# Kernel optimization log

Measured on AMD Instinct MI355X. Metric: run time of the kernel, lower is better.

The kernel has to match this reference:

```python
import jax, jax.numpy as jnp
import numpy as np

EMBED = 512
HEADS = 1
HEAD_DIM = EMBED // HEADS  # 512 (heads must be 1 for the original torch code to run)
N, S = 4, 4096


def setup_inputs() -> dict:
    key = jax.random.key(0)
    ks = jax.random.split(key, 9)
    scale = 1.0 / np.sqrt(EMBED)
    return {
        "values": jax.random.normal(ks[0], (N, 1, S, EMBED), dtype=jnp.float32),
        "keys": jax.random.normal(ks[1], (N, 1, S, EMBED), dtype=jnp.float32),
        "query": jax.random.normal(ks[2], (N, 1, S, EMBED), dtype=jnp.float32),
        "mask": jax.random.randint(ks[3], (N, 1, S, S), 0, 2, dtype=jnp.int32),
        "Wv": jax.random.normal(ks[4], (EMBED, EMBED), dtype=jnp.float32) * scale,
        "Wk": jax.random.normal(ks[5], (EMBED, EMBED), dtype=jnp.float32) * scale,
        "Wq": jax.random.normal(ks[6], (EMBED, EMBED), dtype=jnp.float32) * scale,
        "Wo": jax.random.normal(ks[7], (EMBED, EMBED), dtype=jnp.float32) * scale,
        "bo": jnp.zeros((EMBED,), dtype=jnp.float32),
    }


def reference(values, keys, query, mask, Wv, Wk, Wq, Wo, bo):
    n = query.shape[0]
    q_len = query.shape[2]
    # reshape(N, -1, heads, head_dim); inputs are [N, 1, S, E] -> [N, S, H, Dh]
    v = values.reshape(n, -1, HEADS, HEAD_DIM)
    k = keys.reshape(n, -1, HEADS, HEAD_DIM)
    q = query.reshape(n, -1, HEADS, HEAD_DIM)
    # per-module linear projections (nn.Linear: y = x @ W.T)
    v = jnp.einsum('nlhd,ed->nlhe', v, Wv)
    k = jnp.einsum('nlhd,ed->nlhe', k, Wk)
    q = jnp.einsum('nqhd,ed->nqhe', q, Wq)
    # full [N, H, Q, K] score matrix, as in the original
    energy = jnp.einsum('nqhd,nkhd->nhqk', q, k)
    energy = jnp.where(mask == 0, jnp.float32(-1e20), energy)
    attn = jax.nn.softmax(energy / np.sqrt(HEAD_DIM), axis=3)
    out = jnp.einsum('nhql,nlhd->nqhd', attn, v).reshape(n, q_len, HEADS * HEAD_DIM)
    return out @ Wo.T + bo
```

## Files before the change

kernel.cpp:

```cpp
#include <hip/hip_runtime.h>

typedef __bf16 bf16x8 __attribute__((ext_vector_type(8)));
typedef __bf16 bf16x4 __attribute__((ext_vector_type(4)));
typedef float f32x4 __attribute__((ext_vector_type(4)));
typedef float f32x16 __attribute__((ext_vector_type(16)));

#define MFMA16(a, b, c) __builtin_amdgcn_mfma_f32_16x16x32_bf16((a), (b), (c), 0, 0, 0)
#define MFMA32(a, b, c) __builtin_amdgcn_mfma_f32_32x32x16_bf16((a), (b), (c), 0, 0, 0)

static constexpr int SEQ = 4096;
static constexpr int DIM = 512;

typedef __attribute__((address_space(3))) void lds_void;
typedef __attribute__((address_space(1))) const void gbl_void;

__device__ __forceinline__ void glds16(const void* g, void* l) {
    __builtin_amdgcn_global_load_lds((gbl_void*)g, (lds_void*)l, 16, 0, 0);
}

__device__ __forceinline__ bf16x8 cvt8f(const float* __restrict__ p) {
    float4 f0 = *(const float4*)p;
    float4 f1 = *(const float4*)(p + 4);
    bf16x8 v;
    v[0] = (__bf16)f0.x; v[1] = (__bf16)f0.y; v[2] = (__bf16)f0.z; v[3] = (__bf16)f0.w;
    v[4] = (__bf16)f1.x; v[5] = (__bf16)f1.y; v[6] = (__bf16)f1.z; v[7] = (__bf16)f1.w;
    return v;
}

__global__ __launch_bounds__(256)
void cvt_f32_bf16(const float* __restrict__ in, __bf16* __restrict__ out) {
    const size_t i = ((size_t)blockIdx.x * 256 + threadIdx.x) * 8;
    *(bf16x8*)(out + i) = cvt8f(in + i);
}

__global__ __launch_bounds__(256)
void convert_w(const float* __restrict__ wq, const float* __restrict__ wk,
               const float* __restrict__ wv, const float* __restrict__ wo,
               __bf16* __restrict__ out)
{
    const int z = blockIdx.y;
    const float* src = (z == 0) ? wq : (z == 1) ? wk : (z == 2) ? wv : wo;
    __bf16* dst = out + (size_t)z * DIM * DIM;
    const int i = (blockIdx.x * 256 + threadIdx.x) * 8;
    *(bf16x8*)(dst + i) = cvt8f(src + i);
}

template <bool TRANS>
__global__ __launch_bounds__(256, 3)
void gemm_bf16(const __bf16* __restrict__ Ap, const __bf16* __restrict__ Bp,
               __bf16* __restrict__ Cp)
{
    __shared__ __align__(16) char smem[128 * 132 * 2];
    __bf16* As = (__bf16*)smem;
    __bf16* Bs = (__bf16*)(smem + 16384);

    const int tid  = threadIdx.x;
    const int wave = tid >> 6;
    const int lane = tid & 63;
    const int quad = lane >> 4;
    const int l16  = lane & 15;
    const int m0 = blockIdx.x * 128;
    const int n0 = blockIdx.y * 128;
    const int wm = (wave >> 1) * 64;
    const int wn = (wave & 1) * 64;

    f32x4 acc[4][4] = {};

    for (int k0 = 0; k0 < DIM; k0 += 64) {
        #pragma unroll
        for (int i = 0; i < 4; i++) {
            const int j = wave * 4 + i;
            const int c = j * 64 + lane;
            const int row = c >> 3, c8 = c & 7;
            glds16(Ap + (size_t)(m0 + row) * DIM + k0 + c8 * 8, &As[j * 512]);
            glds16(Bp + (size_t)(n0 + row) * DIM + k0 + c8 * 8, &Bs[j * 512]);
        }
        __syncthreads();
        #pragma unroll
        for (int kk = 0; kk < 2; kk++) {
            bf16x8 af[4], bg[4];
            #pragma unroll
            for (int mt = 0; mt < 4; mt++)
                af[mt] = *(const bf16x8*)&As[(wm + mt * 16 + l16) * 64 + kk * 32 + quad * 8];
            #pragma unroll
            for (int nt = 0; nt < 4; nt++)
                bg[nt] = *(const bf16x8*)&Bs[(wn + nt * 16 + l16) * 64 + kk * 32 + quad * 8];
            #pragma unroll
            for (int mt = 0; mt < 4; mt++)
                #pragma unroll
                for (int nt = 0; nt < 4; nt++)
                    acc[mt][nt] = MFMA16(af[mt], bg[nt], acc[mt][nt]);
        }
        __syncthreads();
    }

    if (!TRANS) {
        #pragma unroll
        for (int mt = 0; mt < 4; mt++)
            #pragma unroll
            for (int nt = 0; nt < 4; nt++)
                #pragma unroll
                for (int r = 0; r < 4; r++)
                    Cp[(size_t)(m0 + wm + mt * 16 + quad * 4 + r) * DIM
                       + n0 + wn + nt * 16 + l16] = (__bf16)acc[mt][nt][r];
    } else {
        __bf16* Tt = (__bf16*)smem;
        #pragma unroll
        for (int mt = 0; mt < 4; mt++)
            #pragma unroll
            for (int nt = 0; nt < 4; nt++)
                #pragma unroll
                for (int r = 0; r < 4; r++)
                    Tt[(wm + mt * 16 + quad * 4 + r) * 132 + wn + nt * 16 + l16]
                        = (__bf16)acc[mt][nt][r];
        __syncthreads();
        const int nb  = m0 >> 12;
        const int s0m = m0 & 4095;
        const int d   = tid >> 1;
        const int sh  = (tid & 1) * 64;
        __bf16* dst = Cp + (size_t)nb * DIM * SEQ + (size_t)(n0 + d) * SEQ + s0m + sh;
        #pragma unroll
        for (int i = 0; i < 8; i++) {
            bf16x8 vv;
            #pragma unroll
            for (int e = 0; e < 8; e++) vv[e] = Tt[(sh + i * 8 + e) * 132 + d];
            *(bf16x8*)(dst + i * 8) = vv;
        }
    }
}

__global__ __launch_bounds__(256, 3)
void gemm_out(const __bf16* __restrict__ Ap, const __bf16* __restrict__ Bp,
              float* __restrict__ Cp, const float* __restrict__ bias)
{
    __shared__ __align__(16) __bf16 As[128 * 64];
    __shared__ __align__(16) __bf16 Bs[128 * 64];
    const int tid  = threadIdx.x;
    const int wave = tid >> 6;
    const int lane = tid & 63;
    const int quad = lane >> 4;
    const int l16  = lane & 15;
    const int m0 = blockIdx.x * 128;
    const int n0 = blockIdx.y * 128;
    const int wm = (wave >> 1) * 64;
    const int wn = (wave & 1) * 64;

    f32x4 acc[4][4] = {};

    for (int k0 = 0; k0 < DIM; k0 += 64) {
        #pragma unroll
        for (int i = 0; i < 4; i++) {
            const int j = wave * 4 + i;
            const int c = j * 64 + lane;
            const int row = c >> 3, c8 = c & 7;
            glds16(Ap + (size_t)(m0 + row) * DIM + k0 + c8 * 8, &As[j * 512]);
            glds16(Bp + (size_t)(n0 + row) * DIM + k0 + c8 * 8, &Bs[j * 512]);
        }
        __syncthreads();
        #pragma unroll
        for (int kk = 0; kk < 2; kk++) {
            bf16x8 af[4], bg[4];
            #pragma unroll
            for (int mt = 0; mt < 4; mt++)
                af[mt] = *(const bf16x8*)&As[(wm + mt * 16 + l16) * 64 + kk * 32 + quad * 8];
            #pragma unroll
            for (int nt = 0; nt < 4; nt++)
                bg[nt] = *(const bf16x8*)&Bs[(wn + nt * 16 + l16) * 64 + kk * 32 + quad * 8];
            #pragma unroll
            for (int mt = 0; mt < 4; mt++)
                #pragma unroll
                for (int nt = 0; nt < 4; nt++)
                    acc[mt][nt] = MFMA16(af[mt], bg[nt], acc[mt][nt]);
        }
        __syncthreads();
    }
    #pragma unroll
    for (int mt = 0; mt < 4; mt++)
        #pragma unroll
        for (int nt = 0; nt < 4; nt++)
            #pragma unroll
            for (int r = 0; r < 4; r++) {
                const int col = n0 + wn + nt * 16 + l16;
                Cp[(size_t)(m0 + wm + mt * 16 + quad * 4 + r) * DIM + col]
                    = acc[mt][nt][r] + bias[col];
            }
}

#define MKC(v, r4) ((r4) == 0 ? (v).x : (r4) == 1 ? (v).y : (r4) == 2 ? (v).z : (v).w)

__global__ __launch_bounds__(512, 1)
void flash_attn(__bf16* __restrict__ Qp, const __bf16* __restrict__ Kp,
                const __bf16* __restrict__ Vt, const int* __restrict__ mask)
{
    constexpr float SCALE = 0.044194173824159216f;

    __shared__ __bf16 KQ[2][20480];
    __shared__ __bf16 P[64 * 256];
    __shared__ float pmax[8 * 66];
    __shared__ float psum[8 * 66];

    const int bid  = blockIdx.x;
    const int n    = bid & 3;
    const int q0   = (bid >> 2) * 64;
    const int tid  = threadIdx.x;
    const int w    = tid >> 6;
    const int lane = tid & 63;
    const int l32  = lane & 31;
    const int half = lane >> 5;
    const int r8   = lane >> 3;
    const int c8   = lane & 7;
    const int gc   = c8 ^ r8;

    const __bf16* Qb = Qp + (size_t)n * SEQ * DIM;
    const __bf16* Kb = Kp + (size_t)n * SEQ * DIM;
    const __bf16* Vb = Vt + (size_t)n * DIM * SEQ;
    const int*    Mb = mask + (size_t)n * SEQ * SEQ;
    __bf16*       AO = Qp + (size_t)n * SEQ * DIM;

    auto stageK = [&](int slot, int k0, int dc) {
        #pragma unroll
        for (int i = 0; i < 4; i++) {
            const int R = (i * 8 + w) * 8 + r8;
            glds16(Kb + (size_t)(k0 + R) * DIM + dc * 64 + gc * 8,
                   &KQ[slot][(i * 8 + w) * 512]);
        }
    };
    auto stageV = [&](int slot, int k0, int vc) {
        const int h = vc >> 2, kc2 = vc & 3;
        #pragma unroll
        for (int i = 0; i < 4; i++) {
            const int R = (i * 8 + w) * 8 + r8;
            glds16(Vb + (size_t)(h * 256 + R) * SEQ + k0 + kc2 * 64 + gc * 8,
                   &KQ[slot][(i * 8 + w) * 512]);
        }
    };
    auto stageQ = [&](int slot, int dc) {
        glds16(Qb + (size_t)(q0 + w * 8 + r8) * DIM + dc * 64 + gc * 8,
               &KQ[slot][16384 + w * 512]);
    };

    float m0 = -__builtin_inff(), m1 = -__builtin_inff();
    float l0 = 0.f, l1 = 0.f;
    f32x16 o00 = {}, o01 = {}, o10 = {}, o11 = {};

    stageK(0, 0, 0);
    stageQ(0, 0);
    __syncthreads();
    int cur = 0;

    #pragma unroll 1
    for (int j = 0; j < 16; j++) {
        const int k0 = j * 256;

        int4 mk0[4], mk1[4];
        {
            const int* mp0 = Mb + (size_t)(q0 + l32) * SEQ + k0 + 32 * w + 4 * half;
            const int* mp1 = mp0 + (size_t)32 * SEQ;
            #pragma unroll
            for (int g = 0; g < 4; g++) {
                mk0[g] = *(const int4*)(mp0 + 8 * g);
                mk1[g] = *(const int4*)(mp1 + 8 * g);
            }
        }

        f32x16 s0 = {}, s1 = {};
        #pragma unroll 1
        for (int dc = 0; dc < 8; dc++) {
            const int nxt = cur ^ 1;
            if (dc < 7) { stageK(nxt, k0, dc + 1); stageQ(nxt, dc + 1); }
            else        { stageV(nxt, k0, 0); }
            const __bf16* Kc = KQ[cur];
            const __bf16* Qc = KQ[cur] + 16384;
            __builtin_amdgcn_s_setprio(1);
            #pragma unroll
            for (int ks = 0; ks < 4; ks++) {
                const int ch = (2 * ks + half) ^ (l32 & 7);
                bf16x8 a  = *(const bf16x8*)&Kc[(32 * w + l32) * 64 + ch * 8];
                bf16x8 b0 = *(const bf16x8*)&Qc[l32 * 64 + ch * 8];
                bf16x8 b1 = *(const bf16x8*)&Qc[(32 + l32) * 64 + ch * 8];
                s0 = MFMA32(a, b0, s0);
                s1 = MFMA32(a, b1, s1);
            }
            __builtin_amdgcn_s_setprio(0);
            if (dc == 7) {
                float mx0 = s0[0], mx1 = s1[0];
                #pragma unroll
                for (int r = 1; r < 16; r++) { mx0 = fmaxf(mx0, s0[r]); mx1 = fmaxf(mx1, s1[r]); }
                mx0 = fmaxf(mx0, __shfl_xor(mx0, 32));
                mx1 = fmaxf(mx1, __shfl_xor(mx1, 32));
                if (half == 0) pmax[w * 66 + l32]      = mx0;
                else           pmax[w * 66 + 32 + l32] = mx1;
            }
            __syncthreads();
            cur = nxt;
        }

        float mp0v = pmax[l32], mp1v = pmax[32 + l32];
        #pragma unroll
        for (int w2 = 1; w2 < 8; w2++) {
            mp0v = fmaxf(mp0v, pmax[w2 * 66 + l32]);
            mp1v = fmaxf(mp1v, pmax[w2 * 66 + 32 + l32]);
        }
        const float mn0 = fmaxf(m0, mp0v * SCALE);
        const float mn1 = fmaxf(m1, mp1v * SCALE);
        const float a0 = __expf(m0 - mn0);
        const float a1 = __expf(m1 - mn1);
        m0 = mn0; m1 = mn1;
        #pragma unroll
        for (int r = 0; r < 16; r++) {
            o00[r] *= a0; o10[r] *= a0;
            o01[r] *= a1; o11[r] *= a1;
        }

        float ls0 = 0.f, ls1 = 0.f;
        #pragma unroll
        for (int g = 0; g < 4; g++) {
            bf16x4 pv0, pv1;
            #pragma unroll
            for (int r4 = 0; r4 < 4; r4++) {
                const int r = g * 4 + r4;
                float p0 = __expf(s0[r] * SCALE - mn0);
                float p1 = __expf(s1[r] * SCALE - mn1);
                p0 = MKC(mk0[g], r4) ? p0 : 0.f;
                p1 = MKC(mk1[g], r4) ? p1 : 0.f;
                ls0 += p0; ls1 += p1;
                pv0[r4] = (__bf16)p0;
                pv1[r4] = (__bf16)p1;
            }
            const int c  = 4 * w + g;
            const int cp = (c & 24) | ((c & 7) ^ (l32 & 7));
            *(bf16x4*)&P[l32 * 256 + cp * 8 + 4 * half]        = pv0;
            *(bf16x4*)&P[(32 + l32) * 256 + cp * 8 + 4 * half] = pv1;
        }
        ls0 += __shfl_xor(ls0, 32);
        ls1 += __shfl_xor(ls1, 32);
        if (half == 0) psum[w * 66 + l32]      = ls0;
        else           psum[w * 66 + 32 + l32] = ls1;
        __syncthreads();

        {
            float ss0 = 0.f, ss1 = 0.f;
            #pragma unroll
            for (int w2 = 0; w2 < 8; w2++) {
                ss0 += psum[w2 * 66 + l32];
                ss1 += psum[w2 * 66 + 32 + l32];
            }
            l0 = l0 * a0 + ss0;
            l1 = l1 * a1 + ss1;
        }

        #pragma unroll 1
        for (int vc = 0; vc < 8; vc++) {
            const int nxt = cur ^ 1;
            if (vc < 7)       stageV(nxt, k0, vc + 1);
            else if (j < 15) { stageK(nxt, k0 + 256, 0); stageQ(nxt, 0); }
            const __bf16* Vc = KQ[cur];
            const int kc2 = vc & 3;
            __builtin_amdgcn_s_setprio(1);
            #pragma unroll
            for (int ks = 0; ks < 4; ks++) {
                const int ca = (2 * ks + half) ^ (l32 & 7);
                bf16x8 a = *(const bf16x8*)&Vc[(32 * w + l32) * 64 + ca * 8];
                const int ck = kc2 * 8 + 2 * ks + half;
                const int cp = (ck & 24) | ((ck & 7) ^ (l32 & 7));
                bf16x8 b0 = *(const bf16x8*)&P[l32 * 256 + cp * 8];
                bf16x8 b1 = *(const bf16x8*)&P[(32 + l32) * 256 + cp * 8];
                if (vc < 4) { o00 = MFMA32(a, b0, o00); o01 = MFMA32(a, b1, o01); }
                else        { o10 = MFMA32(a, b0, o10); o11 = MFMA32(a, b1, o11); }
            }
            __builtin_amdgcn_s_setprio(0);
            __syncthreads();
            cur = nxt;
        }
    }

    const float li0 = 1.f / l0, li1 = 1.f / l1;
    __bf16* ao0 = AO + (size_t)(q0 + l32) * DIM;
    __bf16* ao1 = AO + (size_t)(q0 + 32 + l32) * DIM;
    #pragma unroll
    for (int h = 0; h < 2; h++) {
        #pragma unroll
        for (int g = 0; g < 4; g++) {
            bf16x4 v00, v01;
            #pragma unroll
            for (int r4 = 0; r4 < 4; r4++) {
                const int r = g * 4 + r4;
                v00[r4] = (__bf16)((h ? o10[r] : o00[r]) * li0);
                v01[r4] = (__bf16)((h ? o11[r] : o01[r]) * li1);
            }
            const int d = h * 256 + 32 * w + g * 8 + 4 * half;
            *(bf16x4*)&ao0[d] = v00;
            *(bf16x4*)&ao1[d] = v01;
        }
    }
}

extern "C" void kernel_launch(void* const* d_in, const int* in_sizes, int n_in,
                              void* d_out, int out_size, void* d_ws, size_t ws_size,
                              hipStream_t stream)
{
    const float* values = (const float*)d_in[0];
    const float* keys   = (const float*)d_in[1];
    const float* query  = (const float*)d_in[2];
    const int*   mask   = (const int*)d_in[3];
    const float* Wv = (const float*)d_in[4];
    const float* Wk = (const float*)d_in[5];
    const float* Wq = (const float*)d_in[6];
    const float* Wo = (const float*)d_in[7];
    const float* bo = (const float*)d_in[8];
    float* out = (float*)d_out;

    char* ws = (char*)d_ws;
    __bf16* Qp  = (__bf16*)(ws);
    __bf16* Kp  = (__bf16*)(ws + (16u << 20));
    __bf16* Vt  = (__bf16*)(ws + (32u << 20));
    __bf16* Abf = (__bf16*)(ws + (48u << 20));
    __bf16* wbf = (__bf16*)(ws + (64u << 20));

    const int M = 4 * SEQ;
    const dim3 gg(M / 128, DIM / 128);

    convert_w<<<dim3(128, 4), 256, 0, stream>>>(Wq, Wk, Wv, Wo, wbf);

    cvt_f32_bf16<<<4096, 256, 0, stream>>>(query, Abf);
    gemm_bf16<false><<<gg, 256, 0, stream>>>(Abf, wbf + 0 * DIM * DIM, Qp);

    cvt_f32_bf16<<<4096, 256, 0, stream>>>(keys, Abf);
    gemm_bf16<false><<<gg, 256, 0, stream>>>(Abf, wbf + 1 * DIM * DIM, Kp);

    cvt_f32_bf16<<<4096, 256, 0, stream>>>(values, Abf);
    gemm_bf16<true><<<gg, 256, 0, stream>>>(Abf, wbf + 2 * DIM * DIM, Vt);

    flash_attn<<<256, 512, 0, stream>>>(Qp, Kp, Vt, mask);

    gemm_out<<<gg, 256, 0, stream>>>(Qp , wbf + 3 * DIM * DIM, out, bo);
}
```

Measured before the change: 734.8 us.

## Triple-buffer K/Q/V LDS staging with explicit vmcnt waits and raw barriers

Expands the LDS staging buffer from two to three slots so global-to-LDS loads run two stages ahead of compute. __syncthreads is replaced by explicit s_waitcnt vmcnt counts plus raw s_barrier, so a wave only waits for the oldest outstanding load rather than draining all memory traffic. The V-phase loop is restructured to overlap the first V stage with the row-sum reduction. This uses more LDS and depends on hand-counted vmcnt values, which risks races if the counts are wrong.

```diff
diff --git a/kernel.cpp b/kernel.cpp
--- a/kernel.cpp
+++ b/kernel.cpp
@@ -187,6 +187,9 @@
 }
 
 #define MKC(v, r4) ((r4) == 0 ? (v).x : (r4) == 1 ? (v).y : (r4) == 2 ? (v).z : (v).w)
+#define WAITVM(n)  asm volatile("s_waitcnt vmcnt(" #n ")" ::: "memory")
+#define WAITLGKM() asm volatile("s_waitcnt lgkmcnt(0)" ::: "memory")
+#define BARRIER()  { __builtin_amdgcn_s_barrier(); __builtin_amdgcn_sched_barrier(0); }
 
 __global__ __launch_bounds__(512, 1)
 void flash_attn(__bf16* __restrict__ Qp, const __bf16* __restrict__ Kp,
@@ -194,7 +197,7 @@
 {
     constexpr float SCALE = 0.044194173824159216f;
 
-    __shared__ __bf16 KQ[2][20480];
+    __shared__ __bf16 KQ[3 * 20480];
     __shared__ __bf16 P[64 * 256];
     __shared__ float pmax[8 * 66];
     __shared__ float psum[8 * 66];
@@ -218,34 +221,35 @@
     __bf16*       AO = Qp + (size_t)n * SEQ * DIM;
 
     auto stageK = [&](int slot, int k0, int dc) {
+        __bf16* dst = &KQ[slot * 20480];
         #pragma unroll
         for (int i = 0; i < 4; i++) {
             const int R = (i * 8 + w) * 8 + r8;
             glds16(Kb + (size_t)(k0 + R) * DIM + dc * 64 + gc * 8,
-                   &KQ[slot][(i * 8 + w) * 512]);
+                   &dst[(i * 8 + w) * 512]);
         }
     };
     auto stageV = [&](int slot, int k0, int vc) {
+        __bf16* dst = &KQ[slot * 20480];
         const int h = vc >> 2, kc2 = vc & 3;
         #pragma unroll
         for (int i = 0; i < 4; i++) {
             const int R = (i * 8 + w) * 8 + r8;
             glds16(Vb + (size_t)(h * 256 + R) * SEQ + k0 + kc2 * 64 + gc * 8,
-                   &KQ[slot][(i * 8 + w) * 512]);
+                   &dst[(i * 8 + w) * 512]);
         }
     };
     auto stageQ = [&](int slot, int dc) {
         glds16(Qb + (size_t)(q0 + w * 8 + r8) * DIM + dc * 64 + gc * 8,
-               &KQ[slot][16384 + w * 512]);
+               &KQ[slot * 20480 + 16384 + w * 512]);
     };
 
     float m0 = -__builtin_inff(), m1 = -__builtin_inff();
     float l0 = 0.f, l1 = 0.f;
     f32x16 o00 = {}, o01 = {}, o10 = {}, o11 = {};
 
-    stageK(0, 0, 0);
-    stageQ(0, 0);
-    __syncthreads();
+    stageK(0, 0, 0); stageQ(0, 0);
+    stageK(1, 0, 1); stageQ(1, 1);
     int cur = 0;
 
     #pragma unroll 1
@@ -266,11 +270,17 @@
         f32x16 s0 = {}, s1 = {};
         #pragma unroll 1
         for (int dc = 0; dc < 8; dc++) {
-            const int nxt = cur ^ 1;
-            if (dc < 7) { stageK(nxt, k0, dc + 1); stageQ(nxt, dc + 1); }
-            else        { stageV(nxt, k0, 0); }
-            const __bf16* Kc = KQ[cur];
-            const __bf16* Qc = KQ[cur] + 16384;
+            if (dc < 2)      WAITVM(13);
+            else if (dc < 7) WAITVM(5);
+            else             WAITVM(4);
+            BARRIER();
+            const int s2 = (cur >= 1) ? cur - 1 : cur + 2;
+            if (dc < 6)      { stageK(s2, k0, dc + 2); stageQ(s2, dc + 2); }
+            else if (dc == 6)  stageV(s2, k0, 0);
+            else               stageV(s2, k0, 1);
+
+            const __bf16* Kc = &KQ[cur * 20480];
+            const __bf16* Qc = Kc + 16384;
             __builtin_amdgcn_s_setprio(1);
             #pragma unroll
             for (int ks = 0; ks < 4; ks++) {
@@ -291,9 +301,11 @@
                 if (half == 0) pmax[w * 66 + l32]      = mx0;
                 else           pmax[w * 66 + 32 + l32] = mx1;
             }
-            __syncthreads();
-            cur = nxt;
-        }
+            cur = (cur < 2) ? cur + 1 : 0;
+        }
+
+        WAITLGKM();
+        BARRIER();
 
         float mp0v = pmax[l32], mp1v = pmax[32 + l32];
         #pragma unroll
@@ -336,25 +348,13 @@
         ls1 += __shfl_xor(ls1, 32);
         if (half == 0) psum[w * 66 + l32]      = ls0;
         else           psum[w * 66 + 32 + l32] = ls1;
-        __syncthreads();
-
-        {
-            float ss0 = 0.f, ss1 = 0.f;
-            #pragma unroll
-            for (int w2 = 0; w2 < 8; w2++) {
-                ss0 += psum[w2 * 66 + l32];
-                ss1 += psum[w2 * 66 + 32 + l32];
-            }
-            l0 = l0 * a0 + ss0;
-            l1 = l1 * a1 + ss1;
-        }
-
-        #pragma unroll 1
-        for (int vc = 0; vc < 8; vc++) {
-            const int nxt = cur ^ 1;
-            if (vc < 7)       stageV(nxt, k0, vc + 1);
-            else if (j < 15) { stageK(nxt, k0 + 256, 0); stageQ(nxt, 0); }
-            const __bf16* Vc = KQ[cur];
+
+        WAITVM(4);
+        WAITLGKM();
+        BARRIER();
+
+        auto computeV = [&](int slot, int vc) {
+            const __bf16* Vc = &KQ[slot * 20480];
             const int kc2 = vc & 3;
             __builtin_amdgcn_s_setprio(1);
             #pragma unroll
@@ -369,8 +369,35 @@
                 else        { o10 = MFMA32(a, b0, o10); o11 = MFMA32(a, b1, o11); }
             }
             __builtin_amdgcn_s_setprio(0);
-            __syncthreads();
-            cur = nxt;
+        };
+
+        {
+            const int s2 = (cur >= 1) ? cur - 1 : cur + 2;
+            stageV(s2, k0, 2);
+            float ss0 = 0.f, ss1 = 0.f;
+            #pragma unroll
+            for (int w2 = 0; w2 < 8; w2++) {
+                ss0 += psum[w2 * 66 + l32];
+                ss1 += psum[w2 * 66 + 32 + l32];
+            }
+            l0 = l0 * a0 + ss0;
+            l1 = l1 * a1 + ss1;
+            computeV(cur, 0);
+            cur = (cur < 2) ? cur + 1 : 0;
+        }
+
+        #pragma unroll 1
+        for (int vc = 1; vc < 8; vc++) {
+            if (vc < 7) WAITVM(4);
+            else if (j < 15) WAITVM(5);
+            else WAITVM(0);
+            BARRIER();
+            const int s2 = (cur >= 1) ? cur - 1 : cur + 2;
+            if (vc < 6)        stageV(s2, k0, vc + 2);
+            else if (vc == 6) { if (j < 15) { stageK(s2, k0 + 256, 0); stageQ(s2, 0); } }
+            else              { if (j < 15) { stageK(s2, k0 + 256, 1); stageQ(s2, 1); } }
+            computeV(cur, vc);
+            cur = (cur < 2) ? cur + 1 : 0;
         }
     }
 
```

Result: slower. 820.3 us (+11.6%).

## Fuse fp32-to-bf16 input conversion into a single batched QKV projection GEMM

Applied to the files above, without the earlier changes.

Drops the separate fp32-to-bf16 conversion kernels for query, keys and values. The projection GEMM now reads fp32 activations directly, converts them in registers and writes bf16 into LDS. All three projections run in one launch using blockIdx.z, which removes the intermediate bf16 buffer round-trips and five kernel launches. The cost is that the A-operand loads become synchronous register loads instead of async global-to-LDS loads, and each K tile now reads twice as many A bytes.

```diff
diff --git a/kernel.cpp b/kernel.cpp
--- a/kernel.cpp
+++ b/kernel.cpp
@@ -25,12 +25,6 @@
     v[0] = (__bf16)f0.x; v[1] = (__bf16)f0.y; v[2] = (__bf16)f0.z; v[3] = (__bf16)f0.w;
     v[4] = (__bf16)f1.x; v[5] = (__bf16)f1.y; v[6] = (__bf16)f1.z; v[7] = (__bf16)f1.w;
     return v;
-}
-
-__global__ __launch_bounds__(256)
-void cvt_f32_bf16(const float* __restrict__ in, __bf16* __restrict__ out) {
-    const size_t i = ((size_t)blockIdx.x * 256 + threadIdx.x) * 8;
-    *(bf16x8*)(out + i) = cvt8f(in + i);
 }
 
 __global__ __launch_bounds__(256)
@@ -45,11 +39,17 @@
     *(bf16x8*)(dst + i) = cvt8f(src + i);
 }
 
-template <bool TRANS>
 __global__ __launch_bounds__(256, 3)
-void gemm_bf16(const __bf16* __restrict__ Ap, const __bf16* __restrict__ Bp,
-               __bf16* __restrict__ Cp)
+void gemm_qkv(const float* __restrict__ Aq, const float* __restrict__ Ak,
+              const float* __restrict__ Av, const __bf16* __restrict__ Wb,
+              __bf16* __restrict__ Qp, __bf16* __restrict__ Kp,
+              __bf16* __restrict__ Vtp)
 {
+    const int z = blockIdx.z;
+    const float* Ap = (z == 0) ? Aq : (z == 1) ? Ak : Av;
+    const __bf16* Bp = Wb + (size_t)z * DIM * DIM;
+    __bf16* Cp = (z == 0) ? Qp : (z == 1) ? Kp : Vtp;
+
     __shared__ __align__(16) char smem[128 * 132 * 2];
     __bf16* As = (__bf16*)smem;
     __bf16* Bs = (__bf16*)(smem + 16384);
@@ -70,10 +70,11 @@
         #pragma unroll
         for (int i = 0; i < 4; i++) {
             const int j = wave * 4 + i;
-            const int c = j * 64 + lane;
-            const int row = c >> 3, c8 = c & 7;
-            glds16(Ap + (size_t)(m0 + row) * DIM + k0 + c8 * 8, &As[j * 512]);
+            const int t = j * 64 + lane;
+            const int row = t >> 3, c8 = t & 7;
             glds16(Bp + (size_t)(n0 + row) * DIM + k0 + c8 * 8, &Bs[j * 512]);
+            *(bf16x8*)&As[t * 8] =
+                cvt8f(Ap + (size_t)(m0 + row) * DIM + k0 + c8 * 8);
         }
         __syncthreads();
         #pragma unroll
@@ -94,7 +95,7 @@
         __syncthreads();
     }
 
-    if (!TRANS) {
+    if (z < 2) {
         #pragma unroll
         for (int mt = 0; mt < 4; mt++)
             #pragma unroll
@@ -105,6 +106,7 @@
                        + n0 + wn + nt * 16 + l16] = (__bf16)acc[mt][nt][r];
     } else {
         __bf16* Tt = (__bf16*)smem;
+        __syncthreads();
         #pragma unroll
         for (int mt = 0; mt < 4; mt++)
             #pragma unroll
@@ -414,24 +416,17 @@
     __bf16* Qp  = (__bf16*)(ws);
     __bf16* Kp  = (__bf16*)(ws + (16u << 20));
     __bf16* Vt  = (__bf16*)(ws + (32u << 20));
-    __bf16* Abf = (__bf16*)(ws + (48u << 20));
-    __bf16* wbf = (__bf16*)(ws + (64u << 20));
+    __bf16* wbf = (__bf16*)(ws + (48u << 20));
 
     const int M = 4 * SEQ;
-    const dim3 gg(M / 128, DIM / 128);
 
     convert_w<<<dim3(128, 4), 256, 0, stream>>>(Wq, Wk, Wv, Wo, wbf);
 
-    cvt_f32_bf16<<<4096, 256, 0, stream>>>(query, Abf);
-    gemm_bf16<false><<<gg, 256, 0, stream>>>(Abf, wbf + 0 * DIM * DIM, Qp);
-
-    cvt_f32_bf16<<<4096, 256, 0, stream>>>(keys, Abf);
-    gemm_bf16<false><<<gg, 256, 0, stream>>>(Abf, wbf + 1 * DIM * DIM, Kp);
-
-    cvt_f32_bf16<<<4096, 256, 0, stream>>>(values, Abf);
-    gemm_bf16<true><<<gg, 256, 0, stream>>>(Abf, wbf + 2 * DIM * DIM, Vt);
+    gemm_qkv<<<dim3(M / 128, DIM / 128, 3), 256, 0, stream>>>(
+        query, keys, values, wbf, Qp, Kp, Vt);
 
     flash_attn<<<256, 512, 0, stream>>>(Qp, Kp, Vt, mask);
 
-    gemm_out<<<gg, 256, 0, stream>>>(Qp , wbf + 3 * DIM * DIM, out, bo);
-}
+    gemm_out<<<dim3(M / 128, DIM / 128), 256, 0, stream>>>(
+        Qp , wbf + 3 * DIM * DIM, out, bo);
+}
```

After: 727.3 us. Within noise of the previous version (-1.0%).
